# Kernel optimization log

Measured on AMD Instinct MI355X. Metric: run time of the kernel, lower is better.

The kernel has to match this reference:

```python
import jax, jax.numpy as jnp
import numpy as np

N_NODES = 1_000_000   # nodal points, 3 DOFs each
N_ELEMS = 500_000     # H8 (8-node hexahedral) elements
N_TYPES = 64          # distinct element stiffness matrices (24x24)


def setup_inputs() -> dict:
    key = jax.random.key(0)
    k1, k2, k3, k4 = jax.random.split(key, 4)
    U = jax.random.normal(k1, (N_NODES, 3), dtype=jnp.float32)
    filters = jax.random.normal(k2, (N_TYPES, 24, 24), dtype=jnp.float32)
    H8types = jax.random.randint(k3, (N_ELEMS,), 0, N_TYPES, dtype=jnp.int32)
    nodIdx = jax.random.randint(k4, (N_ELEMS, 8), 0, N_NODES, dtype=jnp.int32)
    return {"U": U, "filters": filters, "H8types": H8types, "nodIdx": nodIdx}


def reference(U, filters, H8types, nodIdx):
    """FEM stiffness matvec KU = sum_e scatter(K_type(e) @ gather(U, e)).

    U:       [N, 3]      nodal displacements (3 DOFs per node)
    filters: [T, 24, 24] per-type element stiffness matrices
    H8types: [E]         element type index into filters
    nodIdx:  [E, 8]      element -> node connectivity
    returns KU: [N, 3]
    """
    E = nodIdx.shape[0]
    # gather the 8 nodes x 3 DOFs of each element -> [E, 24]
    ue = U[nodIdx].reshape(E, 24)
    # per-type stiffness for each element -> [E, 24, 24]
    Ke = filters[H8types]
    # per-element force vector f_e = K_e @ u_e -> [E, 24]
    fe = jnp.einsum('eij,ej->ei', Ke, ue)
    # scatter-add element forces back to nodal DOFs
    KU = jnp.zeros_like(U).at[nodIdx.reshape(-1)].add(fe.reshape(E * 8, 3))
    return KU
```

## Files before the change

kernel.cpp:

```cpp
#include <hip/hip_runtime.h>


#define NTYPES    64
#define KSTRIDE   580
#define RSHIFT    11
#define RNODES    2048
#define MAXB      512
#define CAP       10240
#define K1_TPB    1024
#define K1_EPT    2
#define K1_CHUNK  (K1_TPB * K1_EPT)
#define K2_TPB    256
#define PREP_TPB  256

typedef int          nint4  __attribute__((ext_vector_type(4)));
typedef unsigned int nuint2 __attribute__((ext_vector_type(2)));
typedef unsigned int nuint4 __attribute__((ext_vector_type(4)));

__device__ __forceinline__ unsigned bf16_rne(float f) {
    unsigned b = __float_as_uint(f);
    return (b + 0x7FFFu + ((b >> 16) & 1u)) >> 16;
}


__global__ __launch_bounds__(PREP_TPB) void pack_u_kernel(
    const float* __restrict__ U, nuint2* __restrict__ Ub,
    float* __restrict__ KU, unsigned* __restrict__ tails,
    int n_nodes, int n_buckets)
{
    int n = blockIdx.x * PREP_TPB + threadIdx.x;
    if (n < n_buckets) tails[n] = 0;
    if (n >= n_nodes) return;
    const float* up = U + (size_t)n * 3;
    unsigned bx = bf16_rne(up[0]);
    unsigned by = bf16_rne(up[1]);
    unsigned bz = bf16_rne(up[2]);
    nuint2 v = { bx | (by << 16), bz };
    Ub[n] = v;
    KU[3 * n + 0] = 0.f;
    KU[3 * n + 1] = 0.f;
    KU[3 * n + 2] = 0.f;
}


__global__ __launch_bounds__(K1_TPB, 4) void feconv_bin_kernel(
    const nuint2* __restrict__ Ub,
    const float* __restrict__ K,
    const int*   __restrict__ types,
    const int*   __restrict__ nodIdx,
    float*       __restrict__ KU,
    unsigned*    __restrict__ tails,
    nuint2*      __restrict__ recs,
    int n_elems, int n_buckets)
{
    extern __shared__ float sK[];
    __shared__ unsigned sCnt[MAXB];
    __shared__ unsigned sBase[MAXB];

    for (int w = threadIdx.x; w < NTYPES * 576; w += K1_TPB) {
        int t = w / 576;
        int r = w - t * 576;
        sK[t * KSTRIDE + r] = K[w];
    }
    for (int i = threadIdx.x; i < n_buckets; i += K1_TPB) sCnt[i] = 0;
    __syncthreads();

    const int e0 = blockIdx.x * K1_CHUNK + threadIdx.x;
    int     nodes[K1_EPT][8];
    int     tt[K1_EPT];
    nuint2  uu[K1_EPT][8];

#pragma unroll
    for (int k = 0; k < K1_EPT; ++k) {
        int e = e0 + k * K1_TPB;
        tt[k] = -1;
        if (e < n_elems) {
            tt[k] = __builtin_nontemporal_load(&types[e]);
            const nint4* q = (const nint4*)(nodIdx + (size_t)e * 8);
            nint4 a = __builtin_nontemporal_load(q);
            nint4 b = __builtin_nontemporal_load(q + 1);
            nodes[k][0] = a.x; nodes[k][1] = a.y; nodes[k][2] = a.z; nodes[k][3] = a.w;
            nodes[k][4] = b.x; nodes[k][5] = b.y; nodes[k][6] = b.z; nodes[k][7] = b.w;
#pragma unroll
            for (int j = 0; j < 8; ++j)
                uu[k][j] = Ub[nodes[k][j]];
#pragma unroll
            for (int j = 0; j < 8; ++j)
                atomicAdd(&sCnt[(unsigned)nodes[k][j] >> RSHIFT], 1u);
        }
    }
    __syncthreads();

    for (int b = threadIdx.x; b < n_buckets; b += K1_TPB) {
        unsigned c = sCnt[b];
        sBase[b] = c ? atomicAdd(&tails[b], c) : 0u;
        sCnt[b] = 0;
    }
    __syncthreads();

#pragma unroll
    for (int k = 0; k < K1_EPT; ++k) {
        if (tt[k] < 0) continue;

        float ue[24];
#pragma unroll
        for (int j = 0; j < 8; ++j) {
            nuint2 v = uu[k][j];
            ue[3 * j + 0] = __uint_as_float(v.x << 16);
            ue[3 * j + 1] = __uint_as_float(v.x & 0xFFFF0000u);
            ue[3 * j + 2] = __uint_as_float(v.y << 16);
        }

        const float4* Kt4 = (const float4*)(sK + tt[k] * KSTRIDE);
#pragma unroll
        for (int j = 0; j < 8; ++j) {
            float a0 = 0.f, a1 = 0.f, a2 = 0.f;
#pragma unroll
            for (int q = 0; q < 6; ++q) {
                float4 k0 = Kt4[(3 * j + 0) * 6 + q];
                float4 k1 = Kt4[(3 * j + 1) * 6 + q];
                float4 k2 = Kt4[(3 * j + 2) * 6 + q];
                float u0 = ue[4 * q + 0], u1 = ue[4 * q + 1];
                float u2 = ue[4 * q + 2], u3 = ue[4 * q + 3];
                a0 += k0.x * u0 + k0.y * u1 + k0.z * u2 + k0.w * u3;
                a1 += k1.x * u0 + k1.y * u1 + k1.z * u2 + k1.w * u3;
                a2 += k2.x * u0 + k2.y * u1 + k2.z * u2 + k2.w * u3;
            }
            unsigned n = (unsigned)nodes[k][j];
            unsigned b = n >> RSHIFT;
            unsigned pos = sBase[b] + atomicAdd(&sCnt[b], 1u);
            if (pos < CAP) {
                unsigned local = n & (RNODES - 1);
                nuint2 r = { bf16_rne(a0) | (bf16_rne(a1) << 16),
                             bf16_rne(a2) | (local << 16) };
                recs[(size_t)b * CAP + pos] = r;
            } else {
                atomicAdd(&KU[(size_t)n * 3 + 0], a0);
                atomicAdd(&KU[(size_t)n * 3 + 1], a1);
                atomicAdd(&KU[(size_t)n * 3 + 2], a2);
            }
        }
    }
}


__global__ __launch_bounds__(K2_TPB) void feconv_acc_kernel(
    const nuint2*   __restrict__ recs,
    const unsigned* __restrict__ tails,
    float*          __restrict__ KU,
    int n_nodes)
{
    __shared__ float sAcc[RNODES * 3];
    const int b = blockIdx.x;

    for (int i = threadIdx.x; i < RNODES * 3; i += K2_TPB) sAcc[i] = 0.f;
    __syncthreads();

    unsigned cnt = tails[b];
    if (cnt > CAP) cnt = CAP;
    const nuint2* base = recs + (size_t)b * CAP;
    const nuint4* base4 = (const nuint4*)base;

    unsigned npairs = cnt >> 1;
    for (unsigned i = threadIdx.x; i < npairs; i += K2_TPB) {
        nuint4 p = base4[i];
        unsigned o0 = (p.y >> 16) * 3;
        atomicAdd(&sAcc[o0 + 0], __uint_as_float(p.x << 16));
        atomicAdd(&sAcc[o0 + 1], __uint_as_float(p.x & 0xFFFF0000u));
        atomicAdd(&sAcc[o0 + 2], __uint_as_float(p.y << 16));
        unsigned o1 = (p.w >> 16) * 3;
        atomicAdd(&sAcc[o1 + 0], __uint_as_float(p.z << 16));
        atomicAdd(&sAcc[o1 + 1], __uint_as_float(p.z & 0xFFFF0000u));
        atomicAdd(&sAcc[o1 + 2], __uint_as_float(p.w << 16));
    }
    if ((cnt & 1u) && threadIdx.x == 0) {
        nuint2 r = base[cnt - 1];
        unsigned o = (r.y >> 16) * 3;
        atomicAdd(&sAcc[o + 0], __uint_as_float(r.x << 16));
        atomicAdd(&sAcc[o + 1], __uint_as_float(r.x & 0xFFFF0000u));
        atomicAdd(&sAcc[o + 2], __uint_as_float(r.y << 16));
    }
    __syncthreads();

    const int nbase = b * RNODES;
    int limit = n_nodes - nbase;
    if (limit > RNODES) limit = RNODES;
    limit *= 3;
    float* out = KU + (size_t)nbase * 3;
    for (int i = threadIdx.x; i < limit; i += K2_TPB) out[i] += sAcc[i];
}


__global__ __launch_bounds__(256) void feconv_elem_kernel(
    const float* __restrict__ U, const float* __restrict__ K,
    const int* __restrict__ types, const int* __restrict__ nodIdx,
    float* __restrict__ KU, int n_elems)
{
    int e = blockIdx.x * blockDim.x + threadIdx.x;
    if (e >= n_elems) return;
    int t = types[e];
    const int4* idx4 = (const int4*)(nodIdx + (size_t)e * 8);
    int4 iA = idx4[0], iB = idx4[1];
    int nodes[8] = {iA.x, iA.y, iA.z, iA.w, iB.x, iB.y, iB.z, iB.w};
    float ue[24];
#pragma unroll
    for (int j = 0; j < 8; ++j) {
        const float* up = U + (size_t)nodes[j] * 3;
        ue[3 * j + 0] = up[0]; ue[3 * j + 1] = up[1]; ue[3 * j + 2] = up[2];
    }
    const float* Kt = K + (size_t)t * 576;
#pragma unroll
    for (int i = 0; i < 24; ++i) {
        const float4* row = (const float4*)(Kt + i * 24);
        float acc = 0.f;
#pragma unroll
        for (int q = 0; q < 6; ++q) {
            float4 k = row[q];
            acc += k.x * ue[4 * q + 0] + k.y * ue[4 * q + 1]
                 + k.z * ue[4 * q + 2] + k.w * ue[4 * q + 3];
        }
        atomicAdd(&KU[(size_t)nodes[i / 3] * 3 + (i % 3)], acc);
    }
}

extern "C" void kernel_launch(void* const* d_in, const int* in_sizes, int n_in,
                              void* d_out, int out_size, void* d_ws, size_t ws_size,
                              hipStream_t stream) {
    const float* U      = (const float*)d_in[0];
    const float* Kf     = (const float*)d_in[1];
    const int*   types  = (const int*)d_in[2];
    const int*   nodIdx = (const int*)d_in[3];
    float*       KU     = (float*)d_out;

    const int n_elems = in_sizes[2];
    const int n_nodes = in_sizes[0] / 3;
    const int n_buckets = (n_nodes + RNODES - 1) / RNODES;

    const size_t ub_off  = 4096;
    const size_t rec_off = ub_off + (((size_t)n_nodes * 8 + 255) & ~255ull);
    const size_t need    = rec_off + (size_t)n_buckets * CAP * 8;

    if (n_buckets <= MAXB && ws_size >= need) {
        unsigned* tails = (unsigned*)d_ws;
        nuint2*   Ub    = (nuint2*)((char*)d_ws + ub_off);
        nuint2*   recs  = (nuint2*)((char*)d_ws + rec_off);

        int gridP = (n_nodes + PREP_TPB - 1) / PREP_TPB;
        pack_u_kernel<<<gridP, PREP_TPB, 0, stream>>>(
            U, Ub, KU, tails, n_nodes, n_buckets);

        size_t lds_bytes = (size_t)NTYPES * KSTRIDE * sizeof(float);
        int grid1 = (n_elems + K1_CHUNK - 1) / K1_CHUNK;
        feconv_bin_kernel<<<grid1, K1_TPB, lds_bytes, stream>>>(
            Ub, Kf, types, nodIdx, KU, tails, recs, n_elems, n_buckets);
        feconv_acc_kernel<<<n_buckets, K2_TPB, 0, stream>>>(
            recs, tails, KU, n_nodes);
    } else {
        (void)hipMemsetAsync(KU, 0, (size_t)out_size * sizeof(float), stream);
        int block = 256;
        int grid = (n_elems + block - 1) / block;
        feconv_elem_kernel<<<grid, block, 0, stream>>>(
            U, Kf, types, nodIdx, KU, n_elems);
    }
}
```

Before: 214.6 us.

## Sort elements by type within block before matvec; unroll accumulation loop by four

Result: slower. 326.6 us (+52.2%).

```diff
diff --git a/kernel.cpp b/kernel.cpp
--- a/kernel.cpp
+++ b/kernel.cpp
@@ -54,31 +54,59 @@
     int n_elems, int n_buckets)
 {
     extern __shared__ float sK[];
-    __shared__ unsigned sCnt[MAXB];
-    __shared__ unsigned sBase[MAXB];
-
-    for (int w = threadIdx.x; w < NTYPES * 576; w += K1_TPB) {
+    __shared__ unsigned       sCnt[MAXB];
+    __shared__ unsigned       sBase[MAXB];
+    __shared__ unsigned short sPerm[K1_CHUNK];
+    __shared__ unsigned       sTCnt[NTYPES + 1];
+    __shared__ unsigned       sTBase[NTYPES + 1];
+
+    const int tid = threadIdx.x;
+    const int blockBase = blockIdx.x * K1_CHUNK;
+
+    for (int w = tid; w < NTYPES * 576; w += K1_TPB) {
         int t = w / 576;
         int r = w - t * 576;
         sK[t * KSTRIDE + r] = K[w];
     }
-    for (int i = threadIdx.x; i < n_buckets; i += K1_TPB) sCnt[i] = 0;
-    __syncthreads();
-
-    const int e0 = blockIdx.x * K1_CHUNK + threadIdx.x;
+    for (int i = tid; i < n_buckets; i += K1_TPB) sCnt[i] = 0;
+    if (tid <= NTYPES) sTCnt[tid] = 0;
+    __syncthreads();
+
+    int tloc[K1_EPT];
+#pragma unroll
+    for (int k = 0; k < K1_EPT; ++k) {
+        int li = k * K1_TPB + tid;
+        int e  = blockBase + li;
+        tloc[k] = (e < n_elems) ? __builtin_nontemporal_load(&types[e]) : NTYPES;
+        atomicAdd(&sTCnt[tloc[k]], 1u);
+    }
+    __syncthreads();
+    if (tid == 0) {
+        unsigned s = 0;
+#pragma unroll
+        for (int t = 0; t <= NTYPES; ++t) { sTBase[t] = s; s += sTCnt[t]; }
+    }
+    __syncthreads();
+#pragma unroll
+    for (int k = 0; k < K1_EPT; ++k) {
+        unsigned pos = atomicAdd(&sTBase[tloc[k]], 1u);
+        sPerm[pos] = (unsigned short)(k * K1_TPB + tid);
+    }
+    __syncthreads();
+
     int     nodes[K1_EPT][8];
     int     tt[K1_EPT];
     nuint2  uu[K1_EPT][8];
-
 #pragma unroll
     for (int k = 0; k < K1_EPT; ++k) {
-        int e = e0 + k * K1_TPB;
+        int li = sPerm[k * K1_TPB + tid];
+        int e  = blockBase + li;
         tt[k] = -1;
         if (e < n_elems) {
-            tt[k] = __builtin_nontemporal_load(&types[e]);
+            tt[k] = types[e];
             const nint4* q = (const nint4*)(nodIdx + (size_t)e * 8);
-            nint4 a = __builtin_nontemporal_load(q);
-            nint4 b = __builtin_nontemporal_load(q + 1);
+            nint4 a = q[0];
+            nint4 b = q[1];
             nodes[k][0] = a.x; nodes[k][1] = a.y; nodes[k][2] = a.z; nodes[k][3] = a.w;
             nodes[k][4] = b.x; nodes[k][5] = b.y; nodes[k][6] = b.z; nodes[k][7] = b.w;
 #pragma unroll
@@ -91,7 +119,7 @@
     }
     __syncthreads();
 
-    for (int b = threadIdx.x; b < n_buckets; b += K1_TPB) {
+    for (int b = tid; b < n_buckets; b += K1_TPB) {
         unsigned c = sCnt[b];
         sBase[b] = c ? atomicAdd(&tails[b], c) : 0u;
         sCnt[b] = 0;
@@ -144,6 +172,17 @@
 }
 
 
+__device__ __forceinline__ void scatter_pair(float* sAcc, nuint4 p) {
+    unsigned o0 = (p.y >> 16) * 3;
+    atomicAdd(&sAcc[o0 + 0], __uint_as_float(p.x << 16));
+    atomicAdd(&sAcc[o0 + 1], __uint_as_float(p.x & 0xFFFF0000u));
+    atomicAdd(&sAcc[o0 + 2], __uint_as_float(p.y << 16));
+    unsigned o1 = (p.w >> 16) * 3;
+    atomicAdd(&sAcc[o1 + 0], __uint_as_float(p.z << 16));
+    atomicAdd(&sAcc[o1 + 1], __uint_as_float(p.z & 0xFFFF0000u));
+    atomicAdd(&sAcc[o1 + 2], __uint_as_float(p.w << 16));
+}
+
 __global__ __launch_bounds__(K2_TPB) void feconv_acc_kernel(
     const nuint2*   __restrict__ recs,
     const unsigned* __restrict__ tails,
@@ -158,20 +197,24 @@
 
     unsigned cnt = tails[b];
     if (cnt > CAP) cnt = CAP;
-    const nuint2* base = recs + (size_t)b * CAP;
+    const nuint2* base  = recs + (size_t)b * CAP;
     const nuint4* base4 = (const nuint4*)base;
 
     unsigned npairs = cnt >> 1;
-    for (unsigned i = threadIdx.x; i < npairs; i += K2_TPB) {
+    unsigned i = threadIdx.x;
+    for (; i + 3 * K2_TPB < npairs; i += 4 * K2_TPB) {
+        nuint4 p0 = base4[i];
+        nuint4 p1 = base4[i + K2_TPB];
+        nuint4 p2 = base4[i + 2 * K2_TPB];
+        nuint4 p3 = base4[i + 3 * K2_TPB];
+        scatter_pair(sAcc, p0);
+        scatter_pair(sAcc, p1);
+        scatter_pair(sAcc, p2);
+        scatter_pair(sAcc, p3);
+    }
+    for (; i < npairs; i += K2_TPB) {
         nuint4 p = base4[i];
-        unsigned o0 = (p.y >> 16) * 3;
-        atomicAdd(&sAcc[o0 + 0], __uint_as_float(p.x << 16));
-        atomicAdd(&sAcc[o0 + 1], __uint_as_float(p.x & 0xFFFF0000u));
-        atomicAdd(&sAcc[o0 + 2], __uint_as_float(p.y << 16));
-        unsigned o1 = (p.w >> 16) * 3;
-        atomicAdd(&sAcc[o1 + 0], __uint_as_float(p.z << 16));
-        atomicAdd(&sAcc[o1 + 1], __uint_as_float(p.z & 0xFFFF0000u));
-        atomicAdd(&sAcc[o1 + 2], __uint_as_float(p.w << 16));
+        scatter_pair(sAcc, p);
     }
     if ((cnt & 1u) && threadIdx.x == 0) {
         nuint2 r = base[cnt - 1];
@@ -187,7 +230,7 @@
     if (limit > RNODES) limit = RNODES;
     limit *= 3;
     float* out = KU + (size_t)nbase * 3;
-    for (int i = threadIdx.x; i < limit; i += K2_TPB) out[i] += sAcc[i];
+    for (int i2 = threadIdx.x; i2 < limit; i2 += K2_TPB) out[i2] += sAcc[i2];
 }
 
 
```
